# Performance work log

Measured on AMD Instinct MI355X. Metric: run time of the kernel, lower is better.

The kernel has to match this reference:

```python
import jax, jax.numpy as jnp
import numpy as np

TINY = 1e-30

def fq(x, bits):
    # fake-quantize to `bits` (sign + bits-1 magnitude) with power-of-2 scale,
    # mirroring quant8: q = ceil(log2(max|x|)) - (bits - 2)
    mv = jnp.maximum(jnp.max(jnp.abs(x)), TINY)
    q = jnp.ceil(jnp.log2(mv)) - (bits - 2)
    s = jnp.exp2(q)
    return jnp.round(x / s) * s

def precision_split(x, hi_bits=13, lo_bits=12):
    # PrecisionSplit([13, 12], [16, 16]): hi = 13-bit fake-quant of x,
    # lo = 12-bit fake-quant of the residual. Returns (lo, hi).
    x_hi = fq(x, hi_bits)
    x_lo = fq(x - x_hi, lo_bits)
    return x_lo, x_hi

def gmac_combine(ys, bits=24, bits_headroom=9):
    # GMACv2(24, [1,1,1,1], bits_headroom): align all partial products to a
    # shared power-of-2 accumulator scale (24-bit accumulator with headroom),
    # round, integer-accumulate, rescale.
    mv = jnp.maximum(
        jnp.max(jnp.stack([jnp.max(jnp.abs(y)) for y in ys])), TINY)
    q = jnp.ceil(jnp.log2(mv)) + bits_headroom - (bits - 1)
    s = jnp.exp2(q)
    acc = sum(jnp.round(y / s) for y in ys)
    return acc * s

def setup_inputs() -> dict:
    key = jax.random.key(0)
    kx, kw = jax.random.split(key)
    x = jax.random.normal(kx, (4, 8192, 512), dtype=jnp.float32)
    weight = jax.random.normal(kw, (512, 512), dtype=jnp.float32)  # [d_out, d_in]
    return {"x": x, "weight": weight}

def reference(x, weight):
    # weight split done at __init__ time in the torch module
    w_hi = fq(weight, 8)          # quant8
    w_lo = weight - w_hi
    x_lo, x_hi = precision_split(x)
    # four split-precision matmuls: [B,S,K] @ [K,N]
    y_lo_lo = jnp.matmul(x_lo, w_lo.T)
    y_lo_hi = jnp.matmul(x_lo, w_hi.T)
    y_hi_lo = jnp.matmul(x_hi, w_lo.T)
    y_hi_hi = jnp.matmul(x_hi, w_hi.T)
    return gmac_combine([y_lo_lo, y_lo_hi, y_hi_lo, y_hi_hi],
                        bits=24, bits_headroom=9)
```

## Files before the change

kernel.cpp:

```cpp
#include <hip/hip_runtime.h>
#include <hip/hip_bf16.h>

using f32x4   = __attribute__((ext_vector_type(4))) float;
using bf16x8  = __attribute__((ext_vector_type(8))) short;
using ushort8 = __attribute__((ext_vector_type(8))) unsigned short;

constexpr int N_ = 512;
constexpr int K_ = 512;
constexpr int BM = 128, BN = 128, BK = 64;
constexpr int LDSK = 72;
constexpr int NKS = K_ / BK;

__device__ inline ushort f2bf(float f) {
  union { __hip_bfloat16 h; ushort u; } c;
  c.h = __float2bfloat16(f);
  return c.u;
}

__global__ __launch_bounds__(256)
void pack_w(const float* __restrict__ W, ushort* __restrict__ P) {
  const int tau = blockIdx.x * 256 + threadIdx.x;
  const int l = tau & 63, f = tau >> 6;
  const int row = (f >> 4) * 16 + (l & 15);
  const int kb  = (f & 15) * 32 + (l >> 4) * 8;
  const float* s = W + (size_t)row * K_ + kb;
  f32x4 v0 = *reinterpret_cast<const f32x4*>(s);
  f32x4 v1 = *reinterpret_cast<const f32x4*>(s + 4);
  ushort8 o;
  o[0] = f2bf(v0.x); o[1] = f2bf(v0.y); o[2] = f2bf(v0.z); o[3] = f2bf(v0.w);
  o[4] = f2bf(v1.x); o[5] = f2bf(v1.y); o[6] = f2bf(v1.z); o[7] = f2bf(v1.w);
  *reinterpret_cast<ushort8*>(P + (size_t)tau * 8) = o;
}

__global__ __launch_bounds__(512, 4)
void gemm_pk(const float* __restrict__ X, const ushort* __restrict__ Wp,
             float* __restrict__ C) {
  __shared__ ushort As[2][BM * LDSK];

  const int t    = threadIdx.x;
  const int lane = t & 63;
  const int wave = t >> 6;
  const int wr   = wave >> 1;
  const int wc   = wave & 1;

  const int cpx = gridDim.x >> 3;
  const int bid = (blockIdx.x & 7) * cpx + (blockIdx.x >> 3);
  const int bn  = bid & 3;
  const int bm  = bid >> 2;
  const int m0 = bm * BM, n0 = bn * BN;

  const int sr = t >> 4;
  const int sc = (t & 15) * 4;

  const float* xp = X + (size_t)(m0 + sr) * K_ + sc;
  const ushort* bp = Wp + (size_t)((n0 >> 4) + wc * 4) * 16 * 512 + lane * 8;

  f32x4 acc[2][4] = {};
  f32x4 ra[4];

  auto LOAD = [&](int ks) {
#pragma unroll
    for (int i = 0; i < 4; ++i)
      ra[i] = *reinterpret_cast<const f32x4*>(xp + (size_t)(i * 32) * K_ + ks * BK);
  };

  auto STAGE = [&](ushort* buf) {
#pragma unroll
    for (int i = 0; i < 4; ++i) {
      ushort4 h;
      h.x = f2bf(ra[i].x); h.y = f2bf(ra[i].y);
      h.z = f2bf(ra[i].z); h.w = f2bf(ra[i].w);
      *reinterpret_cast<ushort4*>(&buf[(sr + 32 * i) * LDSK + sc]) = h;
    }
  };

  auto MMA = [&](const ushort* cur, int ks) {
#pragma unroll
    for (int kk = 0; kk < 2; ++kk) {
      const int kc = ks * 2 + kk;
      bf16x8 b0 = *reinterpret_cast<const bf16x8*>(bp + (0 * 16 + kc) * 512);
      bf16x8 b1 = *reinterpret_cast<const bf16x8*>(bp + (1 * 16 + kc) * 512);
      bf16x8 b2 = *reinterpret_cast<const bf16x8*>(bp + (2 * 16 + kc) * 512);
      bf16x8 b3 = *reinterpret_cast<const bf16x8*>(bp + (3 * 16 + kc) * 512);
      const int kof = kk * 32 + (lane >> 4) * 8;
      bf16x8 a0 = *reinterpret_cast<const bf16x8*>(
          &cur[(wr * 32 + 0 * 16 + (lane & 15)) * LDSK + kof]);
      bf16x8 a1 = *reinterpret_cast<const bf16x8*>(
          &cur[(wr * 32 + 1 * 16 + (lane & 15)) * LDSK + kof]);
      acc[0][0] = __builtin_amdgcn_mfma_f32_16x16x32_bf16(a0, b0, acc[0][0], 0, 0, 0);
      acc[0][1] = __builtin_amdgcn_mfma_f32_16x16x32_bf16(a0, b1, acc[0][1], 0, 0, 0);
      acc[0][2] = __builtin_amdgcn_mfma_f32_16x16x32_bf16(a0, b2, acc[0][2], 0, 0, 0);
      acc[0][3] = __builtin_amdgcn_mfma_f32_16x16x32_bf16(a0, b3, acc[0][3], 0, 0, 0);
      acc[1][0] = __builtin_amdgcn_mfma_f32_16x16x32_bf16(a1, b0, acc[1][0], 0, 0, 0);
      acc[1][1] = __builtin_amdgcn_mfma_f32_16x16x32_bf16(a1, b1, acc[1][1], 0, 0, 0);
      acc[1][2] = __builtin_amdgcn_mfma_f32_16x16x32_bf16(a1, b2, acc[1][2], 0, 0, 0);
      acc[1][3] = __builtin_amdgcn_mfma_f32_16x16x32_bf16(a1, b3, acc[1][3], 0, 0, 0);
    }
  };

  ushort* cur = As[0];
  ushort* nxt = As[1];

  LOAD(0);
  STAGE(cur);
  __syncthreads();

  for (int ks = 0; ks < NKS; ++ks) {
    if (ks + 1 < NKS) LOAD(ks + 1);
    MMA(cur, ks);
    if (ks + 1 < NKS) {
      STAGE(nxt);
      ushort* tmp = cur; cur = nxt; nxt = tmp;
      __syncthreads();
    }
  }

  const int col0 = n0 + wc * 64 + (lane & 15);
  const int rsub = (lane >> 4) * 4;
#pragma unroll
  for (int mi = 0; mi < 2; ++mi)
#pragma unroll
    for (int ni = 0; ni < 4; ++ni)
#pragma unroll
      for (int r = 0; r < 4; ++r)
        C[(size_t)(m0 + wr * 32 + mi * 16 + rsub + r) * N_ + (col0 + ni * 16)] =
            acc[mi][ni][r];
}

__global__ __launch_bounds__(512, 4)
void gemm_fb(const float* __restrict__ X, const float* __restrict__ W,
             float* __restrict__ C) {
  __shared__ ushort As[2][BM * LDSK];
  __shared__ ushort Bs[2][BN * LDSK];
  const int t = threadIdx.x, lane = t & 63, wave = t >> 6;
  const int wr = wave >> 2, wc = wave & 3;
  const int cpx = gridDim.x >> 3;
  const int bid = (blockIdx.x & 7) * cpx + (blockIdx.x >> 3);
  const int bn = bid & 3, bm = bid >> 2;
  const int m0 = bm * BM, n0 = bn * BN;
  const int sr = t >> 4, sc = (t & 15) * 4;
  const float* xp = X + (size_t)(m0 + sr) * K_ + sc;
  const float* wp = W + (size_t)(n0 + sr) * K_ + sc;
  f32x4 acc[4][2] = {};
  f32x4 ra[2][4], rb[2][4];
  auto LOAD = [&](int set, int ks) {
#pragma unroll
    for (int i = 0; i < 4; ++i) {
      ra[set][i] = *reinterpret_cast<const f32x4*>(xp + (size_t)(i * 32) * K_ + ks * BK);
      rb[set][i] = *reinterpret_cast<const f32x4*>(wp + (size_t)(i * 32) * K_ + ks * BK);
    }
  };
  auto STAGE = [&](int set, int buf) {
#pragma unroll
    for (int i = 0; i < 4; ++i) {
      ushort4 ha, hb;
      ha.x = f2bf(ra[set][i].x); ha.y = f2bf(ra[set][i].y);
      ha.z = f2bf(ra[set][i].z); ha.w = f2bf(ra[set][i].w);
      hb.x = f2bf(rb[set][i].x); hb.y = f2bf(rb[set][i].y);
      hb.z = f2bf(rb[set][i].z); hb.w = f2bf(rb[set][i].w);
      *reinterpret_cast<ushort4*>(&As[buf][(sr + 32 * i) * LDSK + sc]) = ha;
      *reinterpret_cast<ushort4*>(&Bs[buf][(sr + 32 * i) * LDSK + sc]) = hb;
    }
  };
  auto MMA = [&](int buf) {
#pragma unroll
    for (int kk = 0; kk < 2; ++kk) {
      const int kof = kk * 32 + (lane >> 4) * 8;
      bf16x8 a[4], b[2];
#pragma unroll
      for (int mi = 0; mi < 4; ++mi)
        a[mi] = *reinterpret_cast<const bf16x8*>(
            &As[buf][(wr * 64 + mi * 16 + (lane & 15)) * LDSK + kof]);
#pragma unroll
      for (int ni = 0; ni < 2; ++ni)
        b[ni] = *reinterpret_cast<const bf16x8*>(
            &Bs[buf][(wc * 32 + ni * 16 + (lane & 15)) * LDSK + kof]);
#pragma unroll
      for (int mi = 0; mi < 4; ++mi)
#pragma unroll
        for (int ni = 0; ni < 2; ++ni)
          acc[mi][ni] = __builtin_amdgcn_mfma_f32_16x16x32_bf16(a[mi], b[ni],
                                                                acc[mi][ni], 0, 0, 0);
    }
  };
  LOAD(0, 0); LOAD(1, 1); STAGE(0, 0);
  __syncthreads();
#pragma unroll
  for (int ks = 0; ks < NKS - 1; ++ks) {
    if (ks + 2 < NKS) LOAD(ks & 1, ks + 2);
    MMA(ks & 1);
    STAGE((ks + 1) & 1, (ks + 1) & 1);
    __syncthreads();
  }
  MMA((NKS - 1) & 1);
  const int col0 = n0 + wc * 32 + (lane & 15);
  const int rsub = (lane >> 4) * 4;
#pragma unroll
  for (int mi = 0; mi < 4; ++mi)
#pragma unroll
    for (int ni = 0; ni < 2; ++ni)
#pragma unroll
      for (int r = 0; r < 4; ++r)
        C[(size_t)(m0 + wr * 64 + mi * 16 + rsub + r) * N_ + (col0 + ni * 16)] =
            acc[mi][ni][r];
}

extern "C" void kernel_launch(void* const* d_in, const int* in_sizes, int n_in,
                              void* d_out, int out_size, void* d_ws, size_t ws_size,
                              hipStream_t stream) {
  const float* x = (const float*)d_in[0];
  const float* w = (const float*)d_in[1];
  float* out = (float*)d_out;
  const int M = in_sizes[0] / K_;
  dim3 grid((M / BM) * (N_ / BN));
  if (ws_size >= (size_t)(512 * 1024)) {
    ushort* Wp = (ushort*)d_ws;
    pack_w<<<dim3(128), dim3(256), 0, stream>>>(w, Wp);
    gemm_pk<<<grid, dim3(512), 0, stream>>>(x, Wp, out);
  } else {
    gemm_fb<<<grid, dim3(512), 0, stream>>>(x, w, out);
  }
}
```

Before: 44.04 us.

## Replace LDS-staged packed GEMM with register-direct A loads and narrower N tiles

The packed-weight GEMM no longer stages X through shared memory. Each wave loads its fp32 A fragment directly from global memory in MFMA layout, converts it to bf16 in registers, and double-buffers both A and B fragments with no barriers. The block tile changes from 128x128 with 8 waves to 128x64 with 4 waves, so the grid doubles. This removes LDS traffic and __syncthreads, but X is now read twice from global memory (once per N-tile pair) and the 32-byte strided loads per lane may coalesce less well.

```diff
diff --git a/kernel.cpp b/kernel.cpp
--- a/kernel.cpp
+++ b/kernel.cpp
@@ -7,9 +7,7 @@
 
 constexpr int N_ = 512;
 constexpr int K_ = 512;
-constexpr int BM = 128, BN = 128, BK = 64;
-constexpr int LDSK = 72;
-constexpr int NKS = K_ / BK;
+constexpr int NKC = K_ / 32;
 
 __device__ inline ushort f2bf(float f) {
   union { __hip_bfloat16 h; ushort u; } c;
@@ -32,90 +30,67 @@
   *reinterpret_cast<ushort8*>(P + (size_t)tau * 8) = o;
 }
 
-__global__ __launch_bounds__(512, 4)
-void gemm_pk(const float* __restrict__ X, const ushort* __restrict__ Wp,
-             float* __restrict__ C) {
-  __shared__ ushort As[2][BM * LDSK];
-
+__global__ __launch_bounds__(256, 4)
+void gemm_reg(const float* __restrict__ X, const ushort* __restrict__ Wp,
+              float* __restrict__ C) {
   const int t    = threadIdx.x;
   const int lane = t & 63;
-  const int wave = t >> 6;
-  const int wr   = wave >> 1;
-  const int wc   = wave & 1;
+  const int wr   = t >> 6;
 
   const int cpx = gridDim.x >> 3;
   const int bid = (blockIdx.x & 7) * cpx + (blockIdx.x >> 3);
-  const int bn  = bid & 3;
-  const int bm  = bid >> 2;
-  const int m0 = bm * BM, n0 = bn * BN;
-
-  const int sr = t >> 4;
-  const int sc = (t & 15) * 4;
-
-  const float* xp = X + (size_t)(m0 + sr) * K_ + sc;
-  const ushort* bp = Wp + (size_t)((n0 >> 4) + wc * 4) * 16 * 512 + lane * 8;
-
-  f32x4 acc[2][4] = {};
-  f32x4 ra[4];
-
-  auto LOAD = [&](int ks) {
-#pragma unroll
-    for (int i = 0; i < 4; ++i)
-      ra[i] = *reinterpret_cast<const f32x4*>(xp + (size_t)(i * 32) * K_ + ks * BK);
-  };
-
-  auto STAGE = [&](ushort* buf) {
-#pragma unroll
-    for (int i = 0; i < 4; ++i) {
-      ushort4 h;
-      h.x = f2bf(ra[i].x); h.y = f2bf(ra[i].y);
-      h.z = f2bf(ra[i].z); h.w = f2bf(ra[i].w);
-      *reinterpret_cast<ushort4*>(&buf[(sr + 32 * i) * LDSK + sc]) = h;
-    }
-  };
-
-  auto MMA = [&](const ushort* cur, int ks) {
-#pragma unroll
-    for (int kk = 0; kk < 2; ++kk) {
-      const int kc = ks * 2 + kk;
-      bf16x8 b0 = *reinterpret_cast<const bf16x8*>(bp + (0 * 16 + kc) * 512);
-      bf16x8 b1 = *reinterpret_cast<const bf16x8*>(bp + (1 * 16 + kc) * 512);
-      bf16x8 b2 = *reinterpret_cast<const bf16x8*>(bp + (2 * 16 + kc) * 512);
-      bf16x8 b3 = *reinterpret_cast<const bf16x8*>(bp + (3 * 16 + kc) * 512);
-      const int kof = kk * 32 + (lane >> 4) * 8;
-      bf16x8 a0 = *reinterpret_cast<const bf16x8*>(
-          &cur[(wr * 32 + 0 * 16 + (lane & 15)) * LDSK + kof]);
-      bf16x8 a1 = *reinterpret_cast<const bf16x8*>(
-          &cur[(wr * 32 + 1 * 16 + (lane & 15)) * LDSK + kof]);
-      acc[0][0] = __builtin_amdgcn_mfma_f32_16x16x32_bf16(a0, b0, acc[0][0], 0, 0, 0);
-      acc[0][1] = __builtin_amdgcn_mfma_f32_16x16x32_bf16(a0, b1, acc[0][1], 0, 0, 0);
-      acc[0][2] = __builtin_amdgcn_mfma_f32_16x16x32_bf16(a0, b2, acc[0][2], 0, 0, 0);
-      acc[0][3] = __builtin_amdgcn_mfma_f32_16x16x32_bf16(a0, b3, acc[0][3], 0, 0, 0);
-      acc[1][0] = __builtin_amdgcn_mfma_f32_16x16x32_bf16(a1, b0, acc[1][0], 0, 0, 0);
-      acc[1][1] = __builtin_amdgcn_mfma_f32_16x16x32_bf16(a1, b1, acc[1][1], 0, 0, 0);
-      acc[1][2] = __builtin_amdgcn_mfma_f32_16x16x32_bf16(a1, b2, acc[1][2], 0, 0, 0);
-      acc[1][3] = __builtin_amdgcn_mfma_f32_16x16x32_bf16(a1, b3, acc[1][3], 0, 0, 0);
-    }
-  };
-
-  ushort* cur = As[0];
-  ushort* nxt = As[1];
-
-  LOAD(0);
-  STAGE(cur);
-  __syncthreads();
-
-  for (int ks = 0; ks < NKS; ++ks) {
-    if (ks + 1 < NKS) LOAD(ks + 1);
-    MMA(cur, ks);
-    if (ks + 1 < NKS) {
-      STAGE(nxt);
-      ushort* tmp = cur; cur = nxt; nxt = tmp;
-      __syncthreads();
-    }
+  const int bn  = bid & 7;
+  const int bm  = bid >> 3;
+  const int m0 = bm * 128, n0 = bn * 64;
+
+  const float*  ap = X + (size_t)(m0 + wr * 32 + (lane & 15)) * K_ + ((lane >> 4) * 8);
+  const ushort* bp = Wp + (size_t)(bn * 4) * 16 * 512 + lane * 8;
+
+  f32x4  acc[2][4] = {};
+  f32x4  a[2][2][2];
+  bf16x8 b[2][4];
+
+  auto LDA = [&](int buf, int kc) {
+#pragma unroll
+    for (int mi = 0; mi < 2; ++mi) {
+      const float* p = ap + (size_t)mi * 16 * K_ + kc * 32;
+      a[buf][mi][0] = *reinterpret_cast<const f32x4*>(p);
+      a[buf][mi][1] = *reinterpret_cast<const f32x4*>(p + 4);
+    }
+  };
+  auto LDB = [&](int buf, int kc) {
+#pragma unroll
+    for (int ni = 0; ni < 4; ++ni)
+      b[buf][ni] = *reinterpret_cast<const bf16x8*>(bp + (size_t)(ni * 16 + kc) * 512);
+  };
+
+  LDA(0, 0);
+  LDB(0, 0);
+
+#pragma unroll
+  for (int kc = 0; kc < NKC; ++kc) {
+    const int cur = kc & 1, nxt = cur ^ 1;
+    if (kc + 1 < NKC) { LDA(nxt, kc + 1); LDB(nxt, kc + 1); }
+
+    bf16x8 fa[2];
+#pragma unroll
+    for (int mi = 0; mi < 2; ++mi) {
+      bf16x8 r;
+      r[0] = (short)f2bf(a[cur][mi][0].x); r[1] = (short)f2bf(a[cur][mi][0].y);
+      r[2] = (short)f2bf(a[cur][mi][0].z); r[3] = (short)f2bf(a[cur][mi][0].w);
+      r[4] = (short)f2bf(a[cur][mi][1].x); r[5] = (short)f2bf(a[cur][mi][1].y);
+      r[6] = (short)f2bf(a[cur][mi][1].z); r[7] = (short)f2bf(a[cur][mi][1].w);
+      fa[mi] = r;
+    }
+#pragma unroll
+    for (int mi = 0; mi < 2; ++mi)
+#pragma unroll
+      for (int ni = 0; ni < 4; ++ni)
+        acc[mi][ni] = __builtin_amdgcn_mfma_f32_16x16x32_bf16(fa[mi], b[cur][ni],
+                                                              acc[mi][ni], 0, 0, 0);
   }
 
-  const int col0 = n0 + wc * 64 + (lane & 15);
+  const int col0 = n0 + (lane & 15);
   const int rsub = (lane >> 4) * 4;
 #pragma unroll
   for (int mi = 0; mi < 2; ++mi)
@@ -126,6 +101,10 @@
         C[(size_t)(m0 + wr * 32 + mi * 16 + rsub + r) * N_ + (col0 + ni * 16)] =
             acc[mi][ni][r];
 }
+
+constexpr int BM = 128, BN = 128;
+constexpr int LDSK = 72;
+constexpr int NKS = 8;
 
 __global__ __launch_bounds__(512, 4)
 void gemm_fb(const float* __restrict__ X, const float* __restrict__ W,
@@ -146,8 +125,8 @@
   auto LOAD = [&](int set, int ks) {
 #pragma unroll
     for (int i = 0; i < 4; ++i) {
-      ra[set][i] = *reinterpret_cast<const f32x4*>(xp + (size_t)(i * 32) * K_ + ks * BK);
-      rb[set][i] = *reinterpret_cast<const f32x4*>(wp + (size_t)(i * 32) * K_ + ks * BK);
+      ra[set][i] = *reinterpret_cast<const f32x4*>(xp + (size_t)(i * 32) * K_ + ks * 64);
+      rb[set][i] = *reinterpret_cast<const f32x4*>(wp + (size_t)(i * 32) * K_ + ks * 64);
     }
   };
   auto STAGE = [&](int set, int buf) {
@@ -166,20 +145,20 @@
 #pragma unroll
     for (int kk = 0; kk < 2; ++kk) {
       const int kof = kk * 32 + (lane >> 4) * 8;
-      bf16x8 a[4], b[2];
+      bf16x8 aa[4], bb[2];
 #pragma unroll
       for (int mi = 0; mi < 4; ++mi)
-        a[mi] = *reinterpret_cast<const bf16x8*>(
+        aa[mi] = *reinterpret_cast<const bf16x8*>(
             &As[buf][(wr * 64 + mi * 16 + (lane & 15)) * LDSK + kof]);
 #pragma unroll
       for (int ni = 0; ni < 2; ++ni)
-        b[ni] = *reinterpret_cast<const bf16x8*>(
+        bb[ni] = *reinterpret_cast<const bf16x8*>(
             &Bs[buf][(wc * 32 + ni * 16 + (lane & 15)) * LDSK + kof]);
 #pragma unroll
       for (int mi = 0; mi < 4; ++mi)
 #pragma unroll
         for (int ni = 0; ni < 2; ++ni)
-          acc[mi][ni] = __builtin_amdgcn_mfma_f32_16x16x32_bf16(a[mi], b[ni],
+          acc[mi][ni] = __builtin_amdgcn_mfma_f32_16x16x32_bf16(aa[mi], bb[ni],
                                                                 acc[mi][ni], 0, 0, 0);
     }
   };
@@ -212,12 +191,13 @@
   const float* w = (const float*)d_in[1];
   float* out = (float*)d_out;
   const int M = in_sizes[0] / K_;
-  dim3 grid((M / BM) * (N_ / BN));
   if (ws_size >= (size_t)(512 * 1024)) {
     ushort* Wp = (ushort*)d_ws;
     pack_w<<<dim3(128), dim3(256), 0, stream>>>(w, Wp);
-    gemm_pk<<<grid, dim3(512), 0, stream>>>(x, Wp, out);
+    dim3 grid((M / 128) * (N_ / 64));
+    gemm_reg<<<grid, dim3(256), 0, stream>>>(x, Wp, out);
   } else {
+    dim3 grid((M / 128) * (N_ / 128));
     gemm_fb<<<grid, dim3(512), 0, stream>>>(x, w, out);
   }
 }
```

Measured after the change: 86.36 us. 1.96x slower.

## Deepen A prefetch, preload B fragments per stage, use lightweight barrier

Applied to the files above, without the earlier changes.

The packed-weight GEMM now keeps two register sets of X data, so global loads run two K-stages ahead. The B fragments for the next stage are loaded into registers right after the MMAs instead of inside the MMA loop. The K loop is fully unrolled. __syncthreads is replaced by an explicit lgkmcnt wait plus s_barrier and a sched_barrier, and output stores become nontemporal. These changes aim to hide global-load latency and cut barrier overhead, at the cost of higher register pressure, which may hurt occupancy at 512 threads with 4 waves per SIMD.

```diff
diff --git a/kernel.cpp b/kernel.cpp
--- a/kernel.cpp
+++ b/kernel.cpp
@@ -33,7 +33,7 @@
 }
 
 __global__ __launch_bounds__(512, 4)
-void gemm_pk(const float* __restrict__ X, const ushort* __restrict__ Wp,
+void gemm_v8(const float* __restrict__ X, const ushort* __restrict__ Wp,
              float* __restrict__ C) {
   __shared__ ushort As[2][BM * LDSK];
 
@@ -52,66 +52,77 @@
   const int sr = t >> 4;
   const int sc = (t & 15) * 4;
 
-  const float* xp = X + (size_t)(m0 + sr) * K_ + sc;
+  const float*  xp = X + (size_t)(m0 + sr) * K_ + sc;
   const ushort* bp = Wp + (size_t)((n0 >> 4) + wc * 4) * 16 * 512 + lane * 8;
 
-  f32x4 acc[2][4] = {};
-  f32x4 ra[4];
-
-  auto LOAD = [&](int ks) {
+  f32x4  acc[2][4] = {};
+  f32x4  ra[2][4];
+  bf16x8 b[8];
+
+  auto LOADA = [&](int set, int ks) {
 #pragma unroll
     for (int i = 0; i < 4; ++i)
-      ra[i] = *reinterpret_cast<const f32x4*>(xp + (size_t)(i * 32) * K_ + ks * BK);
-  };
-
-  auto STAGE = [&](ushort* buf) {
+      ra[set][i] = *reinterpret_cast<const f32x4*>(xp + (size_t)(i * 32) * K_ + ks * BK);
+  };
+
+  auto LDB = [&](int ks) {
+#pragma unroll
+    for (int kk = 0; kk < 2; ++kk)
+#pragma unroll
+      for (int ni = 0; ni < 4; ++ni)
+        b[kk * 4 + ni] = *reinterpret_cast<const bf16x8*>(
+            bp + (size_t)(ni * 16 + ks * 2 + kk) * 512);
+  };
+
+  auto STAGE = [&](int set, int buf) {
 #pragma unroll
     for (int i = 0; i < 4; ++i) {
       ushort4 h;
-      h.x = f2bf(ra[i].x); h.y = f2bf(ra[i].y);
-      h.z = f2bf(ra[i].z); h.w = f2bf(ra[i].w);
-      *reinterpret_cast<ushort4*>(&buf[(sr + 32 * i) * LDSK + sc]) = h;
-    }
-  };
-
-  auto MMA = [&](const ushort* cur, int ks) {
+      h.x = f2bf(ra[set][i].x); h.y = f2bf(ra[set][i].y);
+      h.z = f2bf(ra[set][i].z); h.w = f2bf(ra[set][i].w);
+      *reinterpret_cast<ushort4*>(&As[buf][(sr + 32 * i) * LDSK + sc]) = h;
+    }
+  };
+
+  auto MMA = [&](int buf) {
 #pragma unroll
     for (int kk = 0; kk < 2; ++kk) {
-      const int kc = ks * 2 + kk;
-      bf16x8 b0 = *reinterpret_cast<const bf16x8*>(bp + (0 * 16 + kc) * 512);
-      bf16x8 b1 = *reinterpret_cast<const bf16x8*>(bp + (1 * 16 + kc) * 512);
-      bf16x8 b2 = *reinterpret_cast<const bf16x8*>(bp + (2 * 16 + kc) * 512);
-      bf16x8 b3 = *reinterpret_cast<const bf16x8*>(bp + (3 * 16 + kc) * 512);
       const int kof = kk * 32 + (lane >> 4) * 8;
       bf16x8 a0 = *reinterpret_cast<const bf16x8*>(
-          &cur[(wr * 32 + 0 * 16 + (lane & 15)) * LDSK + kof]);
+          &As[buf][(wr * 32 + 0 * 16 + (lane & 15)) * LDSK + kof]);
       bf16x8 a1 = *reinterpret_cast<const bf16x8*>(
-          &cur[(wr * 32 + 1 * 16 + (lane & 15)) * LDSK + kof]);
-      acc[0][0] = __builtin_amdgcn_mfma_f32_16x16x32_bf16(a0, b0, acc[0][0], 0, 0, 0);
-      acc[0][1] = __builtin_amdgcn_mfma_f32_16x16x32_bf16(a0, b1, acc[0][1], 0, 0, 0);
-      acc[0][2] = __builtin_amdgcn_mfma_f32_16x16x32_bf16(a0, b2, acc[0][2], 0, 0, 0);
-      acc[0][3] = __builtin_amdgcn_mfma_f32_16x16x32_bf16(a0, b3, acc[0][3], 0, 0, 0);
-      acc[1][0] = __builtin_amdgcn_mfma_f32_16x16x32_bf16(a1, b0, acc[1][0], 0, 0, 0);
-      acc[1][1] = __builtin_amdgcn_mfma_f32_16x16x32_bf16(a1, b1, acc[1][1], 0, 0, 0);
-      acc[1][2] = __builtin_amdgcn_mfma_f32_16x16x32_bf16(a1, b2, acc[1][2], 0, 0, 0);
-      acc[1][3] = __builtin_amdgcn_mfma_f32_16x16x32_bf16(a1, b3, acc[1][3], 0, 0, 0);
-    }
-  };
-
-  ushort* cur = As[0];
-  ushort* nxt = As[1];
-
-  LOAD(0);
-  STAGE(cur);
-  __syncthreads();
-
+          &As[buf][(wr * 32 + 1 * 16 + (lane & 15)) * LDSK + kof]);
+      acc[0][0] = __builtin_amdgcn_mfma_f32_16x16x32_bf16(a0, b[kk*4+0], acc[0][0], 0, 0, 0);
+      acc[0][1] = __builtin_amdgcn_mfma_f32_16x16x32_bf16(a0, b[kk*4+1], acc[0][1], 0, 0, 0);
+      acc[0][2] = __builtin_amdgcn_mfma_f32_16x16x32_bf16(a0, b[kk*4+2], acc[0][2], 0, 0, 0);
+      acc[0][3] = __builtin_amdgcn_mfma_f32_16x16x32_bf16(a0, b[kk*4+3], acc[0][3], 0, 0, 0);
+      acc[1][0] = __builtin_amdgcn_mfma_f32_16x16x32_bf16(a1, b[kk*4+0], acc[1][0], 0, 0, 0);
+      acc[1][1] = __builtin_amdgcn_mfma_f32_16x16x32_bf16(a1, b[kk*4+1], acc[1][1], 0, 0, 0);
+      acc[1][2] = __builtin_amdgcn_mfma_f32_16x16x32_bf16(a1, b[kk*4+2], acc[1][2], 0, 0, 0);
+      acc[1][3] = __builtin_amdgcn_mfma_f32_16x16x32_bf16(a1, b[kk*4+3], acc[1][3], 0, 0, 0);
+    }
+  };
+
+  auto SYNC = [&]() {
+    asm volatile("s_waitcnt lgkmcnt(0)" ::: "memory");
+    __builtin_amdgcn_s_barrier();
+    __builtin_amdgcn_sched_barrier(0);
+  };
+
+  LOADA(0, 0);
+  LOADA(1, 1);
+  LDB(0);
+  STAGE(0, 0);
+  SYNC();
+
+#pragma unroll
   for (int ks = 0; ks < NKS; ++ks) {
-    if (ks + 1 < NKS) LOAD(ks + 1);
-    MMA(cur, ks);
+    if (ks + 2 < NKS) LOADA(ks & 1, ks + 2);
+    MMA(ks & 1);
     if (ks + 1 < NKS) {
-      STAGE(nxt);
-      ushort* tmp = cur; cur = nxt; nxt = tmp;
-      __syncthreads();
+      LDB(ks + 1);
+      STAGE((ks + 1) & 1, (ks + 1) & 1);
+      SYNC();
     }
   }
 
@@ -123,21 +134,24 @@
     for (int ni = 0; ni < 4; ++ni)
 #pragma unroll
       for (int r = 0; r < 4; ++r)
-        C[(size_t)(m0 + wr * 32 + mi * 16 + rsub + r) * N_ + (col0 + ni * 16)] =
-            acc[mi][ni][r];
-}
+        __builtin_nontemporal_store(
+            acc[mi][ni][r],
+            &C[(size_t)(m0 + wr * 32 + mi * 16 + rsub + r) * N_ + (col0 + ni * 16)]);
+}
+
+constexpr int FBM = 128, FBN = 128, FLDSK = 72, FNKS = 8;
 
 __global__ __launch_bounds__(512, 4)
 void gemm_fb(const float* __restrict__ X, const float* __restrict__ W,
              float* __restrict__ C) {
-  __shared__ ushort As[2][BM * LDSK];
-  __shared__ ushort Bs[2][BN * LDSK];
+  __shared__ ushort Asf[2][FBM * FLDSK];
+  __shared__ ushort Bsf[2][FBN * FLDSK];
   const int t = threadIdx.x, lane = t & 63, wave = t >> 6;
   const int wr = wave >> 2, wc = wave & 3;
   const int cpx = gridDim.x >> 3;
   const int bid = (blockIdx.x & 7) * cpx + (blockIdx.x >> 3);
   const int bn = bid & 3, bm = bid >> 2;
-  const int m0 = bm * BM, n0 = bn * BN;
+  const int m0 = bm * FBM, n0 = bn * FBN;
   const int sr = t >> 4, sc = (t & 15) * 4;
   const float* xp = X + (size_t)(m0 + sr) * K_ + sc;
   const float* wp = W + (size_t)(n0 + sr) * K_ + sc;
@@ -146,8 +160,8 @@
   auto LOAD = [&](int set, int ks) {
 #pragma unroll
     for (int i = 0; i < 4; ++i) {
-      ra[set][i] = *reinterpret_cast<const f32x4*>(xp + (size_t)(i * 32) * K_ + ks * BK);
-      rb[set][i] = *reinterpret_cast<const f32x4*>(wp + (size_t)(i * 32) * K_ + ks * BK);
+      ra[set][i] = *reinterpret_cast<const f32x4*>(xp + (size_t)(i * 32) * K_ + ks * 64);
+      rb[set][i] = *reinterpret_cast<const f32x4*>(wp + (size_t)(i * 32) * K_ + ks * 64);
     }
   };
   auto STAGE = [&](int set, int buf) {
@@ -158,41 +172,41 @@
       ha.z = f2bf(ra[set][i].z); ha.w = f2bf(ra[set][i].w);
       hb.x = f2bf(rb[set][i].x); hb.y = f2bf(rb[set][i].y);
       hb.z = f2bf(rb[set][i].z); hb.w = f2bf(rb[set][i].w);
-      *reinterpret_cast<ushort4*>(&As[buf][(sr + 32 * i) * LDSK + sc]) = ha;
-      *reinterpret_cast<ushort4*>(&Bs[buf][(sr + 32 * i) * LDSK + sc]) = hb;
+      *reinterpret_cast<ushort4*>(&Asf[buf][(sr + 32 * i) * FLDSK + sc]) = ha;
+      *reinterpret_cast<ushort4*>(&Bsf[buf][(sr + 32 * i) * FLDSK + sc]) = hb;
     }
   };
   auto MMA = [&](int buf) {
 #pragma unroll
     for (int kk = 0; kk < 2; ++kk) {
       const int kof = kk * 32 + (lane >> 4) * 8;
-      bf16x8 a[4], b[2];
+      bf16x8 aa[4], bb[2];
 #pragma unroll
       for (int mi = 0; mi < 4; ++mi)
-        a[mi] = *reinterpret_cast<const bf16x8*>(
-            &As[buf][(wr * 64 + mi * 16 + (lane & 15)) * LDSK + kof]);
+        aa[mi] = *reinterpret_cast<const bf16x8*>(
+            &Asf[buf][(wr * 64 + mi * 16 + (lane & 15)) * FLDSK + kof]);
 #pragma unroll
       for (int ni = 0; ni < 2; ++ni)
-        b[ni] = *reinterpret_cast<const bf16x8*>(
-            &Bs[buf][(wc * 32 + ni * 16 + (lane & 15)) * LDSK + kof]);
+        bb[ni] = *reinterpret_cast<const bf16x8*>(
+            &Bsf[buf][(wc * 32 + ni * 16 + (lane & 15)) * FLDSK + kof]);
 #pragma unroll
       for (int mi = 0; mi < 4; ++mi)
 #pragma unroll
         for (int ni = 0; ni < 2; ++ni)
-          acc[mi][ni] = __builtin_amdgcn_mfma_f32_16x16x32_bf16(a[mi], b[ni],
+          acc[mi][ni] = __builtin_amdgcn_mfma_f32_16x16x32_bf16(aa[mi], bb[ni],
                                                                 acc[mi][ni], 0, 0, 0);
     }
   };
   LOAD(0, 0); LOAD(1, 1); STAGE(0, 0);
   __syncthreads();
 #pragma unroll
-  for (int ks = 0; ks < NKS - 1; ++ks) {
-    if (ks + 2 < NKS) LOAD(ks & 1, ks + 2);
+  for (int ks = 0; ks < FNKS - 1; ++ks) {
+    if (ks + 2 < FNKS) LOAD(ks & 1, ks + 2);
     MMA(ks & 1);
     STAGE((ks + 1) & 1, (ks + 1) & 1);
     __syncthreads();
   }
-  MMA((NKS - 1) & 1);
+  MMA((FNKS - 1) & 1);
   const int col0 = n0 + wc * 32 + (lane & 15);
   const int rsub = (lane >> 4) * 4;
 #pragma unroll
@@ -216,7 +230,7 @@
   if (ws_size >= (size_t)(512 * 1024)) {
     ushort* Wp = (ushort*)d_ws;
     pack_w<<<dim3(128), dim3(256), 0, stream>>>(w, Wp);
-    gemm_pk<<<grid, dim3(512), 0, stream>>>(x, Wp, out);
+    gemm_v8<<<grid, dim3(512), 0, stream>>>(x, Wp, out);
   } else {
     gemm_fb<<<grid, dim3(512), 0, stream>>>(x, w, out);
   }
```

Result: slower. 53.95 us (+22.5%).
